# Optimization experiments

Hardware: AMD Instinct MI355X
Metric: run time of the kernel (lower is better)

The kernel has to match this reference:

```python
import jax, jax.numpy as jnp
import numpy as np

B, N, D, H, HID, EN = 2, 4096, 128, 4, 32, 16
ALPHA = 0.2           # LeakyReLU slope
NEG = -9e15           # masked_fill value from the original code


def setup_inputs() -> dict:
    key = jax.random.key(0)
    ks = jax.random.split(key, 6)
    fea = jax.random.normal(ks[0], (B, N, D), dtype=jnp.float32)
    # binary dense adjacency (regulon x gene), square here so narrow() is identity
    adj = jax.random.randint(ks[1], (B, N, N), 0, 2).astype(jnp.float32)
    # per-head GAT params (xavier-ish scale)
    W_heads = jax.random.normal(ks[2], (H, D, HID), dtype=jnp.float32) * 0.1
    a_heads = jax.random.normal(ks[3], (H, 2 * HID, 1), dtype=jnp.float32) * 0.1
    W_last = jax.random.normal(ks[4], (H * HID, EN), dtype=jnp.float32) * 0.1
    a_last = jax.random.normal(ks[5], (2 * EN, 1), dtype=jnp.float32) * 0.1
    return {"fea_mats": fea, "adj_mats": adj, "W_heads": W_heads,
            "a_heads": a_heads, "W_last": W_last, "a_last": a_last}


def _gat_layer(x, adj, W, a, concat):
    # x: [N, d_in], adj: [nr, N], W: [d_in, out], a: [2*out, 1]
    out_dim = W.shape[1]
    wh = x @ W                                   # [N, out]
    nr = adj.shape[0]
    wh1 = wh[:nr] @ a[:out_dim]                  # [nr, 1]
    wh2 = wh @ a[out_dim:]                       # [N, 1]
    e = jax.nn.leaky_relu(wh1 + wh2.T, ALPHA)    # [nr, N]
    # _prepare_attentions: mask by adj, weight by adj, fill zeros with -9e15
    att = jnp.where(adj != 0, e * adj, 0.0)
    att = jnp.where(att == 0, NEG, att)
    att = jax.nn.softmax(att, axis=1)
    # the original detaches attention via a numpy roundtrip
    att = jax.lax.stop_gradient(att)
    res = att @ wh                               # [nr, out]
    return jax.nn.elu(res) if concat else res


def reference(fea_mats, adj_mats, W_heads, a_heads, W_last, a_last):
    def per_sample(x, adj):
        # multi-head attention layers (concat=True), vmapped over heads
        heads = jax.vmap(lambda W, a: _gat_layer(x, adj, W, a, True))(W_heads, a_heads)  # [H, N, HID]
        xcat = jnp.transpose(heads, (1, 0, 2)).reshape(x.shape[0], H * HID)  # torch.cat(dim=1)
        nr = adj.shape[0]
        out = _gat_layer(xcat, adj[:, :nr], W_last, a_last, False)  # adj.narrow(1,0,nr)
        return jax.nn.elu(out)  # [N, EN]
    return jax.vmap(per_sample)(fea_mats, adj_mats)  # [B, N, EN]
```

## Files before the change

### kernel.cpp

```cpp
#include <hip/hip_runtime.h>
#include <hip/hip_bf16.h>
#include <stdint.h>

#define B_ 2
#define N_ 4096
#define D_ 128
#define H_ 4
#define HID_ 32
#define EN_ 16
#define ALPHA_ 0.2f
#define S1_ 4
#define S2_ 4
#define LOG2E_ 1.4426950408889634f

typedef __attribute__((ext_vector_type(8))) _Float16 f16x8;
typedef __attribute__((ext_vector_type(4))) float f32x4;
typedef __attribute__((ext_vector_type(8))) unsigned short u16x8;

__device__ __forceinline__ unsigned short f2h(float v) {
    _Float16 h = (_Float16)v;
    return *(unsigned short*)&h;
}

__global__ __launch_bounds__(256) void prep_kernel(
    const float* __restrict__ adj, unsigned long long* __restrict__ mask,
    const float* __restrict__ fea, const float* __restrict__ Wh,
    const float* __restrict__ a_heads,
    float* __restrict__ wh1, float* __restrict__ wh2,
    float* __restrict__ cmax1, unsigned short* __restrict__ whTt)
{
    __shared__ float xs[32][132];
    __shared__ float WT[32][132];
    __shared__ float Wa[2][128];
    __shared__ float as_[2 * HID_];
    __shared__ unsigned short ts[32][32];
    __shared__ float rmax[32];
    const int tid = threadIdx.x;

    if (blockIdx.x < 2048) {
        const int b = blockIdx.x >> 10, ib = blockIdx.x & 1023;
        const int i = ib * 4 + (tid >> 6);
        const int lane = tid & 63;
        const float* ar = adj + ((size_t)b * N_ + i) * N_;
        unsigned long long* mrow = mask + ((size_t)b * N_ + i) * 64;
#pragma unroll 4
        for (int c = 0; c < 16; ++c) {
            float4 v = *(const float4*)(ar + c * 256 + lane * 4);
            unsigned long long b0 = __ballot(v.x != 0.f);
            unsigned long long b1 = __ballot(v.y != 0.f);
            unsigned long long b2 = __ballot(v.z != 0.f);
            unsigned long long b3 = __ballot(v.w != 0.f);
            if (lane == 0) {
                ulonglong2 w01 = {b0, b1}, w23 = {b2, b3};
                *(ulonglong2*)(mrow + c * 4) = w01;
                *(ulonglong2*)(mrow + c * 4 + 2) = w23;
            }
        }
        return;
    }
    const int l0 = blockIdx.x - 2048;
    const int ib = l0 & 127, h = (l0 >> 7) & 3, b = l0 >> 9;
    const int i0 = ib * 32;
    const float* Wp = Wh + (size_t)h * D_ * HID_;
    for (int l = tid; l < 1024; l += 256) {
        float4 w4 = *(const float4*)(Wp + l * 4);
        int k = l >> 3, d = (l & 7) * 4;
        WT[d][k] = w4.x; WT[d + 1][k] = w4.y; WT[d + 2][k] = w4.z; WT[d + 3][k] = w4.w;
    }
    if (tid < 2 * HID_) as_[tid] = a_heads[h * 2 * HID_ + tid];
    const float* xp = fea + ((size_t)b * N_ + i0) * D_;
    for (int l = tid; l < 1024; l += 256) {
        int r = l >> 5, k4 = (l & 31) * 4;
        *(float4*)&xs[r][k4] = *(const float4*)(xp + r * D_ + k4);
    }
    __syncthreads();
    {
        const int k = tid & 127, j = tid >> 7;
        const float* wr = Wp + k * HID_;
        const float* aw = &as_[j * HID_];
        float s = 0.f;
#pragma unroll
        for (int d = 0; d < HID_; d += 4) {
            float4 w4 = *(const float4*)(wr + d);
            s += w4.x * aw[d] + w4.y * aw[d + 1] + w4.z * aw[d + 2] + w4.w * aw[d + 3];
        }
        Wa[j][k] = s;
    }
    const int c = tid & 15, rg = (tid >> 4) * 2;
    float a0[2] = {0.f, 0.f}, a1[2] = {0.f, 0.f};
#pragma unroll 8
    for (int k = 0; k < D_; k += 4) {
        float4 w0 = *(float4*)&WT[c][k];
        float4 w1 = *(float4*)&WT[c + 16][k];
#pragma unroll
        for (int i = 0; i < 2; ++i) {
            float4 x4 = *(float4*)&xs[rg + i][k];
            a0[i] += x4.x * w0.x + x4.y * w0.y + x4.z * w0.z + x4.w * w0.w;
            a1[i] += x4.x * w1.x + x4.y * w1.y + x4.z * w1.z + x4.w * w1.w;
        }
    }
#pragma unroll
    for (int i = 0; i < 2; ++i) {
        ts[c][rg + i] = f2h(a0[i]);
        ts[c + 16][rg + i] = f2h(a1[i]);
    }
    __syncthreads();
    {
        const int row = tid >> 3, q = tid & 7;
        float d1 = 0.f, d2 = 0.f;
#pragma unroll
        for (int k = q * 16; k < q * 16 + 16; k += 4) {
            float4 x4 = *(float4*)&xs[row][k];
            float4 u = *(float4*)&Wa[0][k];
            float4 v = *(float4*)&Wa[1][k];
            d1 += x4.x * u.x + x4.y * u.y + x4.z * u.z + x4.w * u.w;
            d2 += x4.x * v.x + x4.y * v.y + x4.z * v.z + x4.w * v.w;
        }
        d1 += __shfl_xor(d1, 1); d1 += __shfl_xor(d1, 2); d1 += __shfl_xor(d1, 4);
        d2 += __shfl_xor(d2, 1); d2 += __shfl_xor(d2, 2); d2 += __shfl_xor(d2, 4);
        if (q == 0) {
            const size_t o = (size_t)(b * H_ + h) * N_ + i0 + row;
            wh1[o] = d1 * LOG2E_;
            wh2[o] = d2 * LOG2E_;
            rmax[row] = d2 * LOG2E_;
        }
    }
    __syncthreads();
    if (tid < 128) {
        const int d = tid >> 2, part = (tid & 3) * 8;
        unsigned short* dst = whTt + ((size_t)(b * H_ + h) * 64 + (i0 >> 6)) * 2048
                            + d * 64 + (i0 & 63) + part;
        *(u16x8*)dst = *(u16x8*)&ts[d][part];
    }
    if (tid < 32) {
        float mx = rmax[tid];
#pragma unroll
        for (int off = 16; off; off >>= 1) mx = fmaxf(mx, __shfl_xor(mx, off));
        if (tid == 0) cmax1[(size_t)(b * H_ + h) * 128 + ib] = mx;
    }
}

__global__ __launch_bounds__(256, 4) void attn1_kernel(
    const unsigned long long* __restrict__ mask, const unsigned short* __restrict__ whT,
    const float* __restrict__ wh1, const float* __restrict__ wh2,
    const float* __restrict__ cmax1,
    float* __restrict__ x2p, float* __restrict__ l1p)
{
    __shared__ unsigned long long mask_s[32][17];
    const int b = blockIdx.z, split = blockIdx.y, i0 = blockIdx.x * 32;
    const int tid = threadIdx.x, lane = tid & 63, h = tid >> 6;
    const int m = lane & 15, quad = lane >> 4;
    {
        const int r = tid >> 3, w = (tid & 7) * 2;
        ulonglong2 mw = *(const ulonglong2*)(mask + ((size_t)b * N_ + i0 + r) * 64
                                             + split * 16 + w);
        mask_s[r][w] = mw.x; mask_s[r][w + 1] = mw.y;
    }
    const float* cm = cmax1 + (size_t)(b * H_ + h) * 128;
    float Mh = fmaxf(cm[lane], cm[lane + 64]);
#pragma unroll
    for (int off = 32; off; off >>= 1) Mh = fmaxf(Mh, __shfl_xor(Mh, off));
    const size_t bhN = (size_t)(b * H_ + h) * N_;
    const float w1r0 = wh1[bhN + i0 + m];
    const float w1r1 = wh1[bhN + i0 + 16 + m];
    const float sb0 = w1r0 + Mh, sb1 = w1r1 + Mh;
    const float mr0 = fmaxf(sb0, ALPHA_ * sb0);
    const float mr1 = fmaxf(sb1, ALPHA_ * sb1);
    const float* wvb = wh2 + bhN + split * 1024 + quad * 8;
    const unsigned short* bpb = whT + (size_t)(b * H_ + h) * 131072
                              + (size_t)split * 16 * 2048 + m * 64 + quad * 8;
    f32x4 a00 = {0.f,0.f,0.f,0.f}, a01 = {0.f,0.f,0.f,0.f}, a02 = {0.f,0.f,0.f,0.f};
    f32x4 a10 = {0.f,0.f,0.f,0.f}, a11 = {0.f,0.f,0.f,0.f}, a12 = {0.f,0.f,0.f,0.f};
    f16x8 ones;
#pragma unroll
    for (int q = 0; q < 8; ++q) ones[q] = (_Float16)1.0f;
    __syncthreads();

    for (int c = 0; c < 4; ++c) {
        const unsigned long long P0 = mask_s[m][c*4+0], P1 = mask_s[m][c*4+1];
        const unsigned long long P2 = mask_s[m][c*4+2], P3 = mask_s[m][c*4+3];
        const unsigned long long Q0 = mask_s[m+16][c*4+0], Q1 = mask_s[m+16][c*4+1];
        const unsigned long long Q2 = mask_s[m+16][c*4+2], Q3 = mask_s[m+16][c*4+3];
#pragma unroll
        for (int q4 = 0; q4 < 4; ++q4) {
            const int t = c * 4 + q4;
            const unsigned short* bp = bpb + (size_t)t * 2048;
            f16x8 b00 = *(const f16x8*)bp;
            f16x8 b10 = *(const f16x8*)(bp + 32);
            f16x8 b01 = *(const f16x8*)(bp + 1024);
            f16x8 b11 = *(const f16x8*)(bp + 1056);
            const float* nw = wvb + t * 64;
            float4 u0 = *(const float4*)nw;
            float4 u1 = *(const float4*)(nw + 4);
            float4 v0 = *(const float4*)(nw + 32);
            float4 v1 = *(const float4*)(nw + 36);
#pragma unroll
            for (int ks = 0; ks < 2; ++ks) {
                const int sh = 16 * q4 + 8 * ks + 2 * quad;
                float wv8[8];
                if (ks == 0) { *(float4*)&wv8[0] = u0; *(float4*)&wv8[4] = u1; }
                else         { *(float4*)&wv8[0] = v0; *(float4*)&wv8[4] = v1; }
                const unsigned int gp0 = (unsigned int)(P0 >> sh) & 3u;
                const unsigned int gp1 = (unsigned int)(P1 >> sh) & 3u;
                const unsigned int gp2 = (unsigned int)(P2 >> sh) & 3u;
                const unsigned int gp3 = (unsigned int)(P3 >> sh) & 3u;
                const unsigned int gq0 = (unsigned int)(Q0 >> sh) & 3u;
                const unsigned int gq1 = (unsigned int)(Q1 >> sh) & 3u;
                const unsigned int gq2 = (unsigned int)(Q2 >> sh) & 3u;
                const unsigned int gq3 = (unsigned int)(Q3 >> sh) & 3u;
                f16x8 af0, af1;
#pragma unroll
                for (int qq = 0; qq < 4; ++qq) {
                    float r0p[2], r1p[2];
#pragma unroll
                    for (int cc = 0; cc < 2; ++cc) {
                        const int jj = qq * 2 + cc;
                        const unsigned int bsel = 1u << (jj >> 2);
                        const unsigned int gp = (jj&3)==0?gp0:(jj&3)==1?gp1:(jj&3)==2?gp2:gp3;
                        const unsigned int gq = (jj&3)==0?gq0:(jj&3)==1?gq1:(jj&3)==2?gq2:gq3;
                        float s0 = w1r0 + wv8[jj];
                        float e0 = fmaxf(s0, ALPHA_ * s0);
                        float t0 = ((gp & bsel) == 0u || s0 == 0.f) ? -1e38f : (e0 - mr0);
                        r0p[cc] = __builtin_amdgcn_exp2f(t0);
                        float s1 = w1r1 + wv8[jj];
                        float e1 = fmaxf(s1, ALPHA_ * s1);
                        float t1 = ((gq & bsel) == 0u || s1 == 0.f) ? -1e38f : (e1 - mr1);
                        r1p[cc] = __builtin_amdgcn_exp2f(t1);
                    }
                    auto pr0 = __builtin_amdgcn_cvt_pkrtz(r0p[0], r0p[1]);
                    af0[qq*2] = (_Float16)pr0[0]; af0[qq*2+1] = (_Float16)pr0[1];
                    auto pr1 = __builtin_amdgcn_cvt_pkrtz(r1p[0], r1p[1]);
                    af1[qq*2] = (_Float16)pr1[0]; af1[qq*2+1] = (_Float16)pr1[1];
                }
                f16x8 bb0 = ks ? b10 : b00;
                f16x8 bb1 = ks ? b11 : b01;
                a00 = __builtin_amdgcn_mfma_f32_16x16x32_f16(af0, bb0, a00, 0, 0, 0);
                a01 = __builtin_amdgcn_mfma_f32_16x16x32_f16(af0, bb1, a01, 0, 0, 0);
                a02 = __builtin_amdgcn_mfma_f32_16x16x32_f16(af0, ones, a02, 0, 0, 0);
                a10 = __builtin_amdgcn_mfma_f32_16x16x32_f16(af1, bb0, a10, 0, 0, 0);
                a11 = __builtin_amdgcn_mfma_f32_16x16x32_f16(af1, bb1, a11, 0, 0, 0);
                a12 = __builtin_amdgcn_mfma_f32_16x16x32_f16(af1, ones, a12, 0, 0, 0);
            }
        }
    }
    float* xp = x2p + (((size_t)split * B_ + b) * N_ + i0) * D_ + h * HID_;
#pragma unroll
    for (int reg = 0; reg < 4; ++reg) {
        const int row = quad * 4 + reg;
        xp[(size_t)row * D_ + m] = a00[reg];
        xp[(size_t)row * D_ + 16 + m] = a01[reg];
        xp[(size_t)(row + 16) * D_ + m] = a10[reg];
        xp[(size_t)(row + 16) * D_ + 16 + m] = a11[reg];
    }
    if (m == 0) {
        float* lp = l1p + (((size_t)split * B_ + b) * N_ + i0) * H_ + h;
#pragma unroll
        for (int reg = 0; reg < 4; ++reg) {
            lp[(size_t)(quad * 4 + reg) * H_] = a02[reg];
            lp[(size_t)(quad * 4 + reg + 16) * H_] = a12[reg];
        }
    }
}

__global__ __launch_bounds__(256) void proj2_kernel(
    const float* __restrict__ x2p, const float* __restrict__ l1p,
    const float* __restrict__ Wl, const float* __restrict__ a_last,
    float* __restrict__ wh1b, float* __restrict__ wh2b,
    float* __restrict__ cmax2, unsigned short* __restrict__ whT2t)
{
    __shared__ float Ws[D_ * EN_];
    __shared__ float xs[16][D_];
    __shared__ float as_[2 * EN_];
    __shared__ unsigned short ts[EN_][16];
    __shared__ float rmax[16];
    const int b = blockIdx.y, i0 = blockIdx.x * 16, tid = threadIdx.x;
    for (int idx = tid * 4; idx < D_ * EN_; idx += 1024)
        *(float4*)&Ws[idx] = *(const float4*)(Wl + idx);
    if (tid < 2 * EN_) as_[tid] = a_last[tid];
    for (int idx = tid * 4; idx < 16 * D_; idx += 1024) {
        const int r = idx >> 7, hd = idx & 127, h = hd >> 5;
        float4 v = {0.f, 0.f, 0.f, 0.f};
        float l = 0.f;
#pragma unroll
        for (int s = 0; s < S1_; ++s) {
            const size_t gi = ((size_t)s * B_ + b) * N_ + i0 + r;
            float4 p = *(const float4*)(x2p + gi * D_ + hd);
            v.x += p.x; v.y += p.y; v.z += p.z; v.w += p.w;
            l += l1p[gi * H_ + h];
        }
        float linv = 1.f / fmaxf(l, 1e-30f);
        float o0 = v.x * linv, o1 = v.y * linv, o2 = v.z * linv, o3 = v.w * linv;
        xs[r][hd]     = o0 > 0.f ? o0 : expm1f(o0);
        xs[r][hd + 1] = o1 > 0.f ? o1 : expm1f(o1);
        xs[r][hd + 2] = o2 > 0.f ? o2 : expm1f(o2);
        xs[r][hd + 3] = o3 > 0.f ? o3 : expm1f(o3);
    }
    __syncthreads();
    const int r = tid >> 4, e = tid & 15;
    float acc = 0.f;
#pragma unroll 8
    for (int k = 0; k < D_; ++k) acc += xs[r][k] * Ws[k * EN_ + e];
    ts[e][r] = f2h(acc);
    float d1 = acc * as_[e], d2 = acc * as_[EN_ + e];
#pragma unroll
    for (int off = 8; off; off >>= 1) {
        d1 += __shfl_xor(d1, off);
        d2 += __shfl_xor(d2, off);
    }
    d1 *= LOG2E_; d2 *= LOG2E_;
    if (e == 0) {
        wh1b[(size_t)b * N_ + i0 + r] = d1;
        wh2b[(size_t)b * N_ + i0 + r] = d2;
        rmax[r] = d2;
    }
    __syncthreads();
    if (tid < EN_) {
        unsigned short* dst = whT2t + (size_t)b * 65536
                            + (i0 >> 6) * 1024 + tid * 64 + (i0 & 63);
        *(u16x8*)dst = *(u16x8*)&ts[tid][0];
        *(u16x8*)(dst + 8) = *(u16x8*)&ts[tid][8];
    }
    if (tid == 0) {
        float mx = rmax[0];
#pragma unroll
        for (int k = 1; k < 16; ++k) mx = fmaxf(mx, rmax[k]);
        cmax2[(size_t)b * 256 + blockIdx.x] = mx;
    }
}

__global__ __launch_bounds__(256, 4) void attn2_kernel(
    const unsigned long long* __restrict__ mask, const unsigned short* __restrict__ whT2,
    const float* __restrict__ wh1b, const float* __restrict__ wh2b,
    const float* __restrict__ cmax2,
    float* __restrict__ outp, float* __restrict__ outlp)
{
    __shared__ unsigned long long mask_s[32][17];
    __shared__ float accred[4][32][17];
    __shared__ float lred[4][32];
    const int b = blockIdx.z, split = blockIdx.y, i0 = blockIdx.x * 32;
    const int tid = threadIdx.x, lane = tid & 63, wv = tid >> 6;
    const int m = lane & 15, quad = lane >> 4;
    {
        const int r = tid >> 3, w = (tid & 7) * 2;
        ulonglong2 mw = *(const ulonglong2*)(mask + ((size_t)b * N_ + i0 + r) * 64
                                             + split * 16 + w);
        mask_s[r][w] = mw.x; mask_s[r][w + 1] = mw.y;
    }
    const float* cm = cmax2 + (size_t)b * 256;
    float4 c0 = *(const float4*)(cm + lane * 4);
    float Mh = fmaxf(fmaxf(c0.x, c0.y), fmaxf(c0.z, c0.w));
#pragma unroll
    for (int off = 32; off; off >>= 1) Mh = fmaxf(Mh, __shfl_xor(Mh, off));
    const float w1r0 = wh1b[(size_t)b * N_ + i0 + m];
    const float w1r1 = wh1b[(size_t)b * N_ + i0 + 16 + m];
    const float sb0 = w1r0 + Mh, sb1 = w1r1 + Mh;
    const float mr0 = fmaxf(sb0, ALPHA_ * sb0);
    const float mr1 = fmaxf(sb1, ALPHA_ * sb1);
    const unsigned short* wTb = whT2 + (size_t)b * 65536
                              + (size_t)(split * 16 + wv * 4) * 1024 + m * 64 + quad * 8;
    const float* wvb = wh2b + (size_t)b * N_ + split * 1024 + wv * 256 + quad * 8;
    f32x4 a0 = {0.f,0.f,0.f,0.f}, a1 = {0.f,0.f,0.f,0.f};
    f32x4 l0 = {0.f,0.f,0.f,0.f}, l1 = {0.f,0.f,0.f,0.f};
    f16x8 ones;
#pragma unroll
    for (int q = 0; q < 8; ++q) ones[q] = (_Float16)1.0f;
    __syncthreads();
    const unsigned long long P0 = mask_s[m][wv*4+0], P1 = mask_s[m][wv*4+1];
    const unsigned long long P2 = mask_s[m][wv*4+2], P3 = mask_s[m][wv*4+3];
    const unsigned long long Q0 = mask_s[m+16][wv*4+0], Q1 = mask_s[m+16][wv*4+1];
    const unsigned long long Q2 = mask_s[m+16][wv*4+2], Q3 = mask_s[m+16][wv*4+3];
#pragma unroll
    for (int q4 = 0; q4 < 4; ++q4) {
        const unsigned short* bp = wTb + (size_t)q4 * 1024;
        f16x8 cb0 = *(const f16x8*)(bp);
        f16x8 cb1 = *(const f16x8*)(bp + 32);
        const float* nw = wvb + q4 * 64;
        float4 u0 = *(const float4*)(nw);
        float4 u1 = *(const float4*)(nw + 4);
        float4 v0 = *(const float4*)(nw + 32);
        float4 v1 = *(const float4*)(nw + 36);
#pragma unroll
        for (int ks = 0; ks < 2; ++ks) {
            const int sh = 16 * q4 + 8 * ks + 2 * quad;
            float wv8[8];
            if (ks == 0) { *(float4*)&wv8[0] = u0; *(float4*)&wv8[4] = u1; }
            else         { *(float4*)&wv8[0] = v0; *(float4*)&wv8[4] = v1; }
            const unsigned int gp0 = (unsigned int)(P0 >> sh) & 3u;
            const unsigned int gp1 = (unsigned int)(P1 >> sh) & 3u;
            const unsigned int gp2 = (unsigned int)(P2 >> sh) & 3u;
            const unsigned int gp3 = (unsigned int)(P3 >> sh) & 3u;
            const unsigned int gq0 = (unsigned int)(Q0 >> sh) & 3u;
            const unsigned int gq1 = (unsigned int)(Q1 >> sh) & 3u;
            const unsigned int gq2 = (unsigned int)(Q2 >> sh) & 3u;
            const unsigned int gq3 = (unsigned int)(Q3 >> sh) & 3u;
            f16x8 af0, af1;
#pragma unroll
            for (int qq = 0; qq < 4; ++qq) {
                float r0p[2], r1p[2];
#pragma unroll
                for (int cc = 0; cc < 2; ++cc) {
                    const int jj = qq * 2 + cc;
                    const unsigned int bsel = 1u << (jj >> 2);
                    const unsigned int gp = (jj&3)==0?gp0:(jj&3)==1?gp1:(jj&3)==2?gp2:gp3;
                    const unsigned int gq = (jj&3)==0?gq0:(jj&3)==1?gq1:(jj&3)==2?gq2:gq3;
                    float s0 = w1r0 + wv8[jj];
                    float e0 = fmaxf(s0, ALPHA_ * s0);
                    float t0 = ((gp & bsel) == 0u || s0 == 0.f) ? -1e38f : (e0 - mr0);
                    r0p[cc] = __builtin_amdgcn_exp2f(t0);
                    float s1 = w1r1 + wv8[jj];
                    float e1 = fmaxf(s1, ALPHA_ * s1);
                    float t1 = ((gq & bsel) == 0u || s1 == 0.f) ? -1e38f : (e1 - mr1);
                    r1p[cc] = __builtin_amdgcn_exp2f(t1);
                }
                auto pr0 = __builtin_amdgcn_cvt_pkrtz(r0p[0], r0p[1]);
                af0[qq*2] = (_Float16)pr0[0]; af0[qq*2+1] = (_Float16)pr0[1];
                auto pr1 = __builtin_amdgcn_cvt_pkrtz(r1p[0], r1p[1]);
                af1[qq*2] = (_Float16)pr1[0]; af1[qq*2+1] = (_Float16)pr1[1];
            }
            f16x8 bb = ks ? cb1 : cb0;
            a0 = __builtin_amdgcn_mfma_f32_16x16x32_f16(af0, bb, a0, 0, 0, 0);
            l0 = __builtin_amdgcn_mfma_f32_16x16x32_f16(af0, ones, l0, 0, 0, 0);
            a1 = __builtin_amdgcn_mfma_f32_16x16x32_f16(af1, bb, a1, 0, 0, 0);
            l1 = __builtin_amdgcn_mfma_f32_16x16x32_f16(af1, ones, l1, 0, 0, 0);
        }
    }
#pragma unroll
    for (int reg = 0; reg < 4; ++reg) {
        accred[wv][quad * 4 + reg][m] = a0[reg];
        accred[wv][quad * 4 + reg + 16][m] = a1[reg];
    }
    if (m == 0) {
#pragma unroll
        for (int reg = 0; reg < 4; ++reg) {
            lred[wv][quad * 4 + reg] = l0[reg];
            lred[wv][quad * 4 + reg + 16] = l1[reg];
        }
    }
    __syncthreads();
    const int row = tid >> 4, col = tid & 15;
    float s0 = accred[0][row][col] + accred[1][row][col]
             + accred[2][row][col] + accred[3][row][col];
    float s1 = accred[0][row + 16][col] + accred[1][row + 16][col]
             + accred[2][row + 16][col] + accred[3][row + 16][col];
    float* op = outp + (((size_t)split * B_ + b) * N_ + i0) * EN_;
    op[(size_t)row * EN_ + col] = s0;
    op[(size_t)(row + 16) * EN_ + col] = s1;
    if (tid < 32) {
        float l = lred[0][tid] + lred[1][tid] + lred[2][tid] + lred[3][tid];
        outlp[((size_t)split * B_ + b) * N_ + i0 + tid] = l;
    }
}

__global__ __launch_bounds__(256) void finalize2_kernel(
    const float* __restrict__ outp, const float* __restrict__ outlp,
    float* __restrict__ out)
{
    const int id = blockIdx.x * 256 + threadIdx.x;
    const int gi = id >> 4;
    float num = 0.f, l = 0.f;
#pragma unroll
    for (int s = 0; s < S2_; ++s) {
        num += outp[(size_t)s * B_ * N_ * EN_ + id];
        l   += outlp[(size_t)s * B_ * N_ + gi];
    }
    float v = num / fmaxf(l, 1e-30f);
    out[id] = v > 0.f ? v : expm1f(v);
}

extern "C" void kernel_launch(void* const* d_in, const int* in_sizes, int n_in,
                              void* d_out, int out_size, void* d_ws, size_t ws_size,
                              hipStream_t stream)
{
    const float* fea = (const float*)d_in[0];
    const float* adj = (const float*)d_in[1];
    const float* Wh  = (const float*)d_in[2];
    const float* ah  = (const float*)d_in[3];
    const float* Wl  = (const float*)d_in[4];
    const float* al  = (const float*)d_in[5];

    float* p = (float*)d_ws;
    float* wh1   = p;  p += (size_t)B_ * H_ * N_;
    float* wh2   = p;  p += (size_t)B_ * H_ * N_;
    float* wh1b  = p;  p += (size_t)B_ * N_;
    float* wh2b  = p;  p += (size_t)B_ * N_;
    float* cmax1 = p;  p += (size_t)B_ * H_ * 128;
    float* cmax2 = p;  p += (size_t)B_ * 256;
    float* l1p   = p;  p += (size_t)S1_ * B_ * N_ * H_;
    float* x2p   = p;  p += (size_t)S1_ * B_ * N_ * D_;
    float* outp  = p;  p += (size_t)S2_ * B_ * N_ * EN_;
    float* outlp = p;  p += (size_t)S2_ * B_ * N_;
    unsigned long long* mask = (unsigned long long*)p;
    unsigned short* whTt  = (unsigned short*)(mask + (size_t)B_ * N_ * 64);
    unsigned short* whT2t = whTt + (size_t)B_ * H_ * 131072;

    prep_kernel<<<2048 + B_ * H_ * 128, 256, 0, stream>>>(adj, mask, fea, Wh, ah,
                                                          wh1, wh2, cmax1, whTt);
    attn1_kernel<<<dim3(N_ / 32, S1_, B_), 256, 0, stream>>>(mask, whTt, wh1, wh2, cmax1,
                                                             x2p, l1p);
    proj2_kernel<<<dim3(N_ / 16, B_), 256, 0, stream>>>(x2p, l1p, Wl, al,
                                                        wh1b, wh2b, cmax2, whT2t);
    attn2_kernel<<<dim3(N_ / 32, S2_, B_), 256, 0, stream>>>(mask, whT2t, wh1b, wh2b, cmax2,
                                                             outp, outlp);
    finalize2_kernel<<<(B_ * N_ * EN_) / 256, 256, 0, stream>>>(outp, outlp, (float*)d_out);
}
```

Before: 282.8 us.

## Fuse second attention layer split-K reduction and finalize into one kernel

Removes the four-way column split of the second attention layer. Each 512-thread block now covers all 4096 columns for 32 rows, with 8 waves each handling two chunks. The wave partials are reduced in shared memory, and the normalize and ELU are applied in the same kernel. This drops the finalize kernel launch and the partial-buffer round trip through global memory. In exchange, the grid shrinks from 1024 to 256 blocks, which lowers parallelism and each block does more serial work.

```diff
diff --git a/kernel.cpp b/kernel.cpp
--- a/kernel.cpp
+++ b/kernel.cpp
@@ -10,7 +10,6 @@
 #define EN_ 16
 #define ALPHA_ 0.2f
 #define S1_ 4
-#define S2_ 4
 #define LOG2E_ 1.4426950408889634f
 
 typedef __attribute__((ext_vector_type(8))) _Float16 f16x8;
@@ -328,23 +327,24 @@
     }
 }
 
-__global__ __launch_bounds__(256, 4) void attn2_kernel(
+__global__ __launch_bounds__(512) void attn2f_kernel(
     const unsigned long long* __restrict__ mask, const unsigned short* __restrict__ whT2,
     const float* __restrict__ wh1b, const float* __restrict__ wh2b,
-    const float* __restrict__ cmax2,
-    float* __restrict__ outp, float* __restrict__ outlp)
+    const float* __restrict__ cmax2, float* __restrict__ out)
 {
-    __shared__ unsigned long long mask_s[32][17];
-    __shared__ float accred[4][32][17];
-    __shared__ float lred[4][32];
-    const int b = blockIdx.z, split = blockIdx.y, i0 = blockIdx.x * 32;
+    __shared__ unsigned long long mask_s[32][66];
+    __shared__ float accred[8][32][17];
+    __shared__ float lred[8][32];
+    const int b = blockIdx.y, i0 = blockIdx.x * 32;
     const int tid = threadIdx.x, lane = tid & 63, wv = tid >> 6;
     const int m = lane & 15, quad = lane >> 4;
     {
-        const int r = tid >> 3, w = (tid & 7) * 2;
-        ulonglong2 mw = *(const ulonglong2*)(mask + ((size_t)b * N_ + i0 + r) * 64
-                                             + split * 16 + w);
-        mask_s[r][w] = mw.x; mask_s[r][w + 1] = mw.y;
+        const int r = tid >> 4, w = (tid & 15) * 4;
+        const unsigned long long* src = mask + ((size_t)b * N_ + i0 + r) * 64 + w;
+        ulonglong2 m0 = *(const ulonglong2*)src;
+        ulonglong2 m1 = *(const ulonglong2*)(src + 2);
+        mask_s[r][w] = m0.x; mask_s[r][w + 1] = m0.y;
+        mask_s[r][w + 2] = m1.x; mask_s[r][w + 3] = m1.y;
     }
     const float* cm = cmax2 + (size_t)b * 256;
     float4 c0 = *(const float4*)(cm + lane * 4);
@@ -356,72 +356,77 @@
     const float sb0 = w1r0 + Mh, sb1 = w1r1 + Mh;
     const float mr0 = fmaxf(sb0, ALPHA_ * sb0);
     const float mr1 = fmaxf(sb1, ALPHA_ * sb1);
-    const unsigned short* wTb = whT2 + (size_t)b * 65536
-                              + (size_t)(split * 16 + wv * 4) * 1024 + m * 64 + quad * 8;
-    const float* wvb = wh2b + (size_t)b * N_ + split * 1024 + wv * 256 + quad * 8;
+    const unsigned short* wTg = whT2 + (size_t)b * 65536 + m * 64 + quad * 8;
+    const float* w2g = wh2b + (size_t)b * N_ + quad * 8;
     f32x4 a0 = {0.f,0.f,0.f,0.f}, a1 = {0.f,0.f,0.f,0.f};
     f32x4 l0 = {0.f,0.f,0.f,0.f}, l1 = {0.f,0.f,0.f,0.f};
     f16x8 ones;
 #pragma unroll
     for (int q = 0; q < 8; ++q) ones[q] = (_Float16)1.0f;
     __syncthreads();
-    const unsigned long long P0 = mask_s[m][wv*4+0], P1 = mask_s[m][wv*4+1];
-    const unsigned long long P2 = mask_s[m][wv*4+2], P3 = mask_s[m][wv*4+3];
-    const unsigned long long Q0 = mask_s[m+16][wv*4+0], Q1 = mask_s[m+16][wv*4+1];
-    const unsigned long long Q2 = mask_s[m+16][wv*4+2], Q3 = mask_s[m+16][wv*4+3];
-#pragma unroll
-    for (int q4 = 0; q4 < 4; ++q4) {
-        const unsigned short* bp = wTb + (size_t)q4 * 1024;
-        f16x8 cb0 = *(const f16x8*)(bp);
-        f16x8 cb1 = *(const f16x8*)(bp + 32);
-        const float* nw = wvb + q4 * 64;
-        float4 u0 = *(const float4*)(nw);
-        float4 u1 = *(const float4*)(nw + 4);
-        float4 v0 = *(const float4*)(nw + 32);
-        float4 v1 = *(const float4*)(nw + 36);
-#pragma unroll
-        for (int ks = 0; ks < 2; ++ks) {
-            const int sh = 16 * q4 + 8 * ks + 2 * quad;
-            float wv8[8];
-            if (ks == 0) { *(float4*)&wv8[0] = u0; *(float4*)&wv8[4] = u1; }
-            else         { *(float4*)&wv8[0] = v0; *(float4*)&wv8[4] = v1; }
-            const unsigned int gp0 = (unsigned int)(P0 >> sh) & 3u;
-            const unsigned int gp1 = (unsigned int)(P1 >> sh) & 3u;
-            const unsigned int gp2 = (unsigned int)(P2 >> sh) & 3u;
-            const unsigned int gp3 = (unsigned int)(P3 >> sh) & 3u;
-            const unsigned int gq0 = (unsigned int)(Q0 >> sh) & 3u;
-            const unsigned int gq1 = (unsigned int)(Q1 >> sh) & 3u;
-            const unsigned int gq2 = (unsigned int)(Q2 >> sh) & 3u;
-            const unsigned int gq3 = (unsigned int)(Q3 >> sh) & 3u;
-            f16x8 af0, af1;
-#pragma unroll
-            for (int qq = 0; qq < 4; ++qq) {
-                float r0p[2], r1p[2];
-#pragma unroll
-                for (int cc = 0; cc < 2; ++cc) {
-                    const int jj = qq * 2 + cc;
-                    const unsigned int bsel = 1u << (jj >> 2);
-                    const unsigned int gp = (jj&3)==0?gp0:(jj&3)==1?gp1:(jj&3)==2?gp2:gp3;
-                    const unsigned int gq = (jj&3)==0?gq0:(jj&3)==1?gq1:(jj&3)==2?gq2:gq3;
-                    float s0 = w1r0 + wv8[jj];
-                    float e0 = fmaxf(s0, ALPHA_ * s0);
-                    float t0 = ((gp & bsel) == 0u || s0 == 0.f) ? -1e38f : (e0 - mr0);
-                    r0p[cc] = __builtin_amdgcn_exp2f(t0);
-                    float s1 = w1r1 + wv8[jj];
-                    float e1 = fmaxf(s1, ALPHA_ * s1);
-                    float t1 = ((gq & bsel) == 0u || s1 == 0.f) ? -1e38f : (e1 - mr1);
-                    r1p[cc] = __builtin_amdgcn_exp2f(t1);
+
+#pragma unroll
+    for (int cc = 0; cc < 2; ++cc) {
+        const int ch = wv * 2 + cc;
+        const unsigned long long P0 = mask_s[m][ch*4+0], P1 = mask_s[m][ch*4+1];
+        const unsigned long long P2 = mask_s[m][ch*4+2], P3 = mask_s[m][ch*4+3];
+        const unsigned long long Q0 = mask_s[m+16][ch*4+0], Q1 = mask_s[m+16][ch*4+1];
+        const unsigned long long Q2 = mask_s[m+16][ch*4+2], Q3 = mask_s[m+16][ch*4+3];
+#pragma unroll
+        for (int q4 = 0; q4 < 4; ++q4) {
+            const int jb = ch * 4 + q4;
+            const unsigned short* bp = wTg + (size_t)jb * 1024;
+            f16x8 cb0 = *(const f16x8*)(bp);
+            f16x8 cb1 = *(const f16x8*)(bp + 32);
+            const float* nw = w2g + jb * 64;
+            float4 u0 = *(const float4*)(nw);
+            float4 u1 = *(const float4*)(nw + 4);
+            float4 v0 = *(const float4*)(nw + 32);
+            float4 v1 = *(const float4*)(nw + 36);
+#pragma unroll
+            for (int ks = 0; ks < 2; ++ks) {
+                const int sh = 16 * q4 + 8 * ks + 2 * quad;
+                float wv8[8];
+                if (ks == 0) { *(float4*)&wv8[0] = u0; *(float4*)&wv8[4] = u1; }
+                else         { *(float4*)&wv8[0] = v0; *(float4*)&wv8[4] = v1; }
+                const unsigned int gp0 = (unsigned int)(P0 >> sh) & 3u;
+                const unsigned int gp1 = (unsigned int)(P1 >> sh) & 3u;
+                const unsigned int gp2 = (unsigned int)(P2 >> sh) & 3u;
+                const unsigned int gp3 = (unsigned int)(P3 >> sh) & 3u;
+                const unsigned int gq0 = (unsigned int)(Q0 >> sh) & 3u;
+                const unsigned int gq1 = (unsigned int)(Q1 >> sh) & 3u;
+                const unsigned int gq2 = (unsigned int)(Q2 >> sh) & 3u;
+                const unsigned int gq3 = (unsigned int)(Q3 >> sh) & 3u;
+                f16x8 af0, af1;
+#pragma unroll
+                for (int qq = 0; qq < 4; ++qq) {
+                    float r0p[2], r1p[2];
+#pragma unroll
+                    for (int c2 = 0; c2 < 2; ++c2) {
+                        const int jj = qq * 2 + c2;
+                        const unsigned int bsel = 1u << (jj >> 2);
+                        const unsigned int gp = (jj&3)==0?gp0:(jj&3)==1?gp1:(jj&3)==2?gp2:gp3;
+                        const unsigned int gq = (jj&3)==0?gq0:(jj&3)==1?gq1:(jj&3)==2?gq2:gq3;
+                        float s0 = w1r0 + wv8[jj];
+                        float e0 = fmaxf(s0, ALPHA_ * s0);
+                        float t0 = ((gp & bsel) == 0u || s0 == 0.f) ? -1e38f : (e0 - mr0);
+                        r0p[c2] = __builtin_amdgcn_exp2f(t0);
+                        float s1 = w1r1 + wv8[jj];
+                        float e1 = fmaxf(s1, ALPHA_ * s1);
+                        float t1 = ((gq & bsel) == 0u || s1 == 0.f) ? -1e38f : (e1 - mr1);
+                        r1p[c2] = __builtin_amdgcn_exp2f(t1);
+                    }
+                    auto pr0 = __builtin_amdgcn_cvt_pkrtz(r0p[0], r0p[1]);
+                    af0[qq*2] = (_Float16)pr0[0]; af0[qq*2+1] = (_Float16)pr0[1];
+                    auto pr1 = __builtin_amdgcn_cvt_pkrtz(r1p[0], r1p[1]);
+                    af1[qq*2] = (_Float16)pr1[0]; af1[qq*2+1] = (_Float16)pr1[1];
                 }
-                auto pr0 = __builtin_amdgcn_cvt_pkrtz(r0p[0], r0p[1]);
-                af0[qq*2] = (_Float16)pr0[0]; af0[qq*2+1] = (_Float16)pr0[1];
-                auto pr1 = __builtin_amdgcn_cvt_pkrtz(r1p[0], r1p[1]);
-                af1[qq*2] = (_Float16)pr1[0]; af1[qq*2+1] = (_Float16)pr1[1];
+                f16x8 bb = ks ? cb1 : cb0;
+                a0 = __builtin_amdgcn_mfma_f32_16x16x32_f16(af0, bb, a0, 0, 0, 0);
+                l0 = __builtin_amdgcn_mfma_f32_16x16x32_f16(af0, ones, l0, 0, 0, 0);
+                a1 = __builtin_amdgcn_mfma_f32_16x16x32_f16(af1, bb, a1, 0, 0, 0);
+                l1 = __builtin_amdgcn_mfma_f32_16x16x32_f16(af1, ones, l1, 0, 0, 0);
             }
-            f16x8 bb = ks ? cb1 : cb0;
-            a0 = __builtin_amdgcn_mfma_f32_16x16x32_f16(af0, bb, a0, 0, 0, 0);
-            l0 = __builtin_amdgcn_mfma_f32_16x16x32_f16(af0, ones, l0, 0, 0, 0);
-            a1 = __builtin_amdgcn_mfma_f32_16x16x32_f16(af1, bb, a1, 0, 0, 0);
-            l1 = __builtin_amdgcn_mfma_f32_16x16x32_f16(af1, ones, l1, 0, 0, 0);
         }
     }
 #pragma unroll
@@ -438,33 +443,11 @@
     }
     __syncthreads();
     const int row = tid >> 4, col = tid & 15;
-    float s0 = accred[0][row][col] + accred[1][row][col]
-             + accred[2][row][col] + accred[3][row][col];
-    float s1 = accred[0][row + 16][col] + accred[1][row + 16][col]
-             + accred[2][row + 16][col] + accred[3][row + 16][col];
-    float* op = outp + (((size_t)split * B_ + b) * N_ + i0) * EN_;
-    op[(size_t)row * EN_ + col] = s0;
-    op[(size_t)(row + 16) * EN_ + col] = s1;
-    if (tid < 32) {
-        float l = lred[0][tid] + lred[1][tid] + lred[2][tid] + lred[3][tid];
-        outlp[((size_t)split * B_ + b) * N_ + i0 + tid] = l;
-    }
-}
-
-__global__ __launch_bounds__(256) void finalize2_kernel(
-    const float* __restrict__ outp, const float* __restrict__ outlp,
-    float* __restrict__ out)
-{
-    const int id = blockIdx.x * 256 + threadIdx.x;
-    const int gi = id >> 4;
-    float num = 0.f, l = 0.f;
-#pragma unroll
-    for (int s = 0; s < S2_; ++s) {
-        num += outp[(size_t)s * B_ * N_ * EN_ + id];
-        l   += outlp[(size_t)s * B_ * N_ + gi];
-    }
-    float v = num / fmaxf(l, 1e-30f);
-    out[id] = v > 0.f ? v : expm1f(v);
+    float s = 0.f, l = 0.f;
+#pragma unroll
+    for (int w = 0; w < 8; ++w) { s += accred[w][row][col]; l += lred[w][row]; }
+    float v = s / fmaxf(l, 1e-30f);
+    out[((size_t)b * N_ + i0 + row) * EN_ + col] = v > 0.f ? v : expm1f(v);
 }
 
 extern "C" void kernel_launch(void* const* d_in, const int* in_sizes, int n_in,
@@ -487,8 +470,6 @@
     float* cmax2 = p;  p += (size_t)B_ * 256;
     float* l1p   = p;  p += (size_t)S1_ * B_ * N_ * H_;
     float* x2p   = p;  p += (size_t)S1_ * B_ * N_ * D_;
-    float* outp  = p;  p += (size_t)S2_ * B_ * N_ * EN_;
-    float* outlp = p;  p += (size_t)S2_ * B_ * N_;
     unsigned long long* mask = (unsigned long long*)p;
     unsigned short* whTt  = (unsigned short*)(mask + (size_t)B_ * N_ * 64);
     unsigned short* whT2t = whTt + (size_t)B_ * H_ * 131072;
@@ -499,7 +480,6 @@
                                                              x2p, l1p);
     proj2_kernel<<<dim3(N_ / 16, B_), 256, 0, stream>>>(x2p, l1p, Wl, al,
                                                         wh1b, wh2b, cmax2, whT2t);
-    attn2_kernel<<<dim3(N_ / 32, S2_, B_), 256, 0, stream>>>(mask, whT2t, wh1b, wh2b, cmax2,
-                                                             outp, outlp);
-    finalize2_kernel<<<(B_ * N_ * EN_) / 256, 256, 0, stream>>>(outp, outlp, (float*)d_out);
-}
+    attn2f_kernel<<<dim3(N_ / 32, B_), 512, 0, stream>>>(mask, whT2t, wh1b, wh2b, cmax2,
+                                                         (float*)d_out);
+}
```

Measured after the change: 284.4 us. Within noise of the previous version (+0.6%).
